# Optimization experiments

Measured on AMD Instinct MI355X. Metric: run time of the kernel, lower is better.

The kernel has to match this reference:

```python
import jax, jax.numpy as jnp
from jax import lax
import numpy as np

T, B, DIM_F, DIM_H, DIM_S, DIM_W = 1024, 32, 512, 512, 1024, 512


def setup_inputs() -> dict:
    key = jax.random.key(0)
    ks = jax.random.split(key, 9)
    F_matrix = jax.random.normal(ks[0], (T, DIM_F), dtype=jnp.float32)
    a_prev = jax.nn.softmax(jax.random.normal(ks[1], (B, T), dtype=jnp.float32), axis=1)
    s_prev = jax.random.normal(ks[2], (B, DIM_S), dtype=jnp.float32)
    h = jax.random.normal(ks[3], (T, B, DIM_H), dtype=jnp.float32)
    # Linear weights stored as [in, out] so y = x @ W (+ b)
    Ww = jax.random.normal(ks[4], (DIM_S, DIM_W), dtype=jnp.float32) / np.sqrt(DIM_S)
    Vw = jax.random.normal(ks[5], (DIM_H, DIM_W), dtype=jnp.float32) / np.sqrt(DIM_H)
    Vb = jax.random.normal(ks[6], (DIM_W,), dtype=jnp.float32) * 0.01
    Uw = jax.random.normal(ks[7], (DIM_F, DIM_W), dtype=jnp.float32) / np.sqrt(DIM_F)
    ww = jax.random.normal(ks[8], (DIM_W,), dtype=jnp.float32) / np.sqrt(DIM_W)
    return {"F_matrix": F_matrix, "a_prev": a_prev, "s_prev": s_prev, "h": h,
            "Ww": Ww, "Vw": Vw, "Vb": Vb, "Uw": Uw, "ww": ww, "beta": 1}


def _calc_f(F_matrix, a_prev):
    # torch.conv2d(input=[1,1,T,dim_f], weight=[B,1,T,1], padding=[(T-1)//2, 0])
    t = F_matrix.shape[0]
    pad = (t - 1) // 2
    lhs = F_matrix[None, None]          # [1, 1, T, dim_f]
    rhs = a_prev[:, None, :, None]      # [B, 1, T, 1]
    f = lax.conv_general_dilated(
        lhs, rhs, window_strides=(1, 1), padding=[(pad, pad), (0, 0)],
        dimension_numbers=("NCHW", "OIHW", "NCHW"))[0]  # [B, T_out, dim_f]
    if f.shape[1] != t:  # even T -> T_out = T-1; pad one leading time row with zeros
        f = jnp.pad(f, ((0, 0), (1, 0), (0, 0)))
    return f


def reference(F_matrix, a_prev, s_prev, h, Ww, Vw, Vb, Uw, ww, beta):
    f_current = _calc_f(F_matrix, a_prev)                 # [B, T, dim_f]
    hT = jnp.swapaxes(h, 0, 1)                            # [B, T, dim_h]
    x = jnp.tanh(jnp.matmul(s_prev, Ww)[:, None, :]       # Ws: [B, 1, dim_w]
                 + jnp.matmul(hT, Vw) + Vb                # Vh: [B, T, dim_w]
                 + jnp.matmul(f_current, Uw))             # Uf: [B, T, dim_w]
    e_current = jnp.einsum("btw,w->bt", x, ww)            # [B, T]
    return jax.nn.softmax(beta * e_current, axis=1)       # 'sharpening' mode
```

## Files before the change

### kernel.cpp

```cpp
#include <hip/hip_runtime.h>
#include <hip/hip_bf16.h>
#include <math.h>

#define T_DIM 1024
#define B_DIM 32
#define DIMF 512
#define DIMH 512
#define DIMS 1024
#define DIMW 512

typedef __attribute__((ext_vector_type(8))) short short8;
typedef __attribute__((ext_vector_type(4))) float f32x4;

__device__ __forceinline__ unsigned f2bf1(float x) {
    unsigned a = __float_as_uint(x);
    return (a + 0x7FFFu + ((a >> 16) & 1u)) >> 16;
}
__device__ __forceinline__ unsigned f2bf2(float lo, float hi) {
    return f2bf1(lo) | (f2bf1(hi) << 16);
}
__device__ __forceinline__ float fast_tanh(float x) {
    return 1.f - __fdividef(2.f, 1.f + __expf(x + x));
}
__device__ __forceinline__ unsigned short bf1(float x) {
    __hip_bfloat16 b = __float2bfloat16(x);
    return *reinterpret_cast<unsigned short*>(&b);
}
__device__ __forceinline__ short8 pack8(float4 a, float4 c) {
    union { unsigned short us[8]; short8 s; } u;
    u.us[0] = bf1(a.x); u.us[1] = bf1(a.y); u.us[2] = bf1(a.z); u.us[3] = bf1(a.w);
    u.us[4] = bf1(c.x); u.us[5] = bf1(c.y); u.us[6] = bf1(c.z); u.us[7] = bf1(c.w);
    return u.s;
}

__device__ __forceinline__ void gl16(const unsigned short* g, unsigned short* l) {
    __builtin_amdgcn_global_load_lds(
        (const __attribute__((address_space(1))) unsigned int*)g,
        (__attribute__((address_space(3))) unsigned int*)l, 16, 0, 0);
}
__device__ __forceinline__ void gl16f(const float* g, float* l) {
    __builtin_amdgcn_global_load_lds(
        (const __attribute__((address_space(1))) unsigned int*)g,
        (__attribute__((address_space(3))) unsigned int*)l, 16, 0, 0);
}

__global__ void __launch_bounds__(256) k_prep_all(
    const float* __restrict__ F, const float* __restrict__ Uw,
    const float* __restrict__ Vw, const float* __restrict__ a_prev,
    const float* __restrict__ s_prev, const float* __restrict__ Ww,
    const float* __restrict__ Vb, const float* __restrict__ h,
    unsigned short* __restrict__ GT, unsigned short* __restrict__ VwT,
    unsigned short* __restrict__ P, float* __restrict__ SWp,
    unsigned short* __restrict__ hB, int nPack) {
    __shared__ float sh[8192];
    const int bz = blockIdx.x;
    const int tid = threadIdx.x;

    if (bz < nPack) {
        for (unsigned i = bz * 256 + tid; i < 32768u * 64; i += (unsigned)nPack * 256) {
            const int r = i >> 6, c8 = (i & 63) * 8;
            const int bb = r >> 10, t = r & 1023;
            const float* src = h + ((size_t)(t * 32 + bb)) * 512 + c8;
            const float4 v0 = *(const float4*)(src);
            const float4 v1 = *(const float4*)(src + 4);
            union { unsigned short us[8]; uint4 u4; } o;
            o.us[0] = bf1(v0.x); o.us[1] = bf1(v0.y);
            o.us[2] = bf1(v0.z); o.us[3] = bf1(v0.w);
            o.us[4] = bf1(v1.x); o.us[5] = bf1(v1.y);
            o.us[6] = bf1(v1.z); o.us[7] = bf1(v1.w);
            *(uint4*)(hB + (size_t)r * 512 + c8) = o.u4;
        }
        return;
    }
    const int bz2 = bz - nPack;
    if (bz2 < 512) {
        const int rt = bz2 & 63, ct = bz2 >> 6;
        const int r0g = rt * 16;
        const float4* Fv = (const float4*)(F + (size_t)r0g * DIMF);
        float4* shv = (float4*)sh;
        for (int i = tid; i < 16 * DIMF / 4; i += 256) shv[i] = Fv[i];
        __syncthreads();
        const int c = ct * 64 + (tid & 63);
        const int r0 = (tid >> 6) * 4;
        float acc[4] = {0.f, 0.f, 0.f, 0.f};
        for (int k = 0; k < DIMF; ++k) {
            const float bv = Uw[(size_t)k * DIMW + c];
#pragma unroll
            for (int j = 0; j < 4; ++j)
                acc[j] = fmaf(sh[(r0 + j) * DIMF + k], bv, acc[j]);
        }
        uint2 o;
        o.x = f2bf2(acc[0], acc[1]);
        o.y = f2bf2(acc[2], acc[3]);
        *(uint2*)(GT + (size_t)c * T_DIM + r0g + r0) = o;
        return;
    }
    const int bz3 = bz2 - 512;
    if (bz3 < 512) {
        if (bz3 < 256) {
            const int k0 = (bz3 >> 4) * 32, n0 = (bz3 & 15) * 32;
            const int x = tid & 31, y = tid >> 5;
#pragma unroll
            for (int i = 0; i < 4; ++i)
                sh[(y + 8 * i) * 33 + x] = Vw[(size_t)(k0 + y + 8 * i) * DIMW + n0 + x];
            __syncthreads();
#pragma unroll
            for (int i = 0; i < 4; ++i) {
                const int n = n0 + y + 8 * i;
                VwT[(size_t)n * DIMH + k0 + x] = (unsigned short)f2bf1(sh[x * 33 + y + 8 * i]);
            }
        } else {
            const int bs = bz3 - 256;
            const int b = bs >> 3, s = bs & 7;
            for (int i = tid; i < 2048; i += 256) {
                const int j = i + s;
                float v = 0.f;
                if (j >= 512 && j < 1536) v = a_prev[(size_t)b * T_DIM + j - 512];
                P[(size_t)bs * 2048 + i] = (unsigned short)f2bf1(v);
            }
        }
        return;
    }
    {
        const int bz4 = bz3 - 512;
        const int c0 = (bz4 & 15) * 32, q = bz4 >> 4;
        float (*shb)[256] = (float(*)[256])sh;
        for (int i = tid; i < 32 * 64; i += 256) {
            const int r = i >> 6, c4 = (i & 63) * 4;
            *(float4*)&shb[r][c4] = *(const float4*)(s_prev + (size_t)r * DIMS + q * 256 + c4);
        }
        __syncthreads();
        const int c  = c0 + (tid & 31);
        const int bg = tid >> 5;
        float acc[4];
#pragma unroll
        for (int j = 0; j < 4; ++j) acc[j] = (q == 0) ? Vb[c] : 0.f;
        const float* W = Ww + (size_t)q * 256 * DIMW;
        for (int k = 0; k < 256; ++k) {
            const float w = W[(size_t)k * DIMW + c];
#pragma unroll
            for (int j = 0; j < 4; ++j)
                acc[j] = fmaf(shb[bg + 8 * j][k], w, acc[j]);
        }
#pragma unroll
        for (int j = 0; j < 4; ++j)
            SWp[((size_t)q * B_DIM + bg + 8 * j) * DIMW + c] = acc[j];
    }
}

__global__ void __launch_bounds__(512, 4) k_main_db(
    const unsigned short* __restrict__ hB, const unsigned short* __restrict__ VwT,
    const unsigned short* __restrict__ GT, const unsigned short* __restrict__ P,
    const float* __restrict__ SWp, const float* __restrict__ ww,
    float* __restrict__ ep) {
    __shared__ unsigned short As2[2][8192];
    __shared__ unsigned short Bs[2][8192];

    const int bid = blockIdx.x;
    const int wg  = (bid & 7) * 128 + (bid >> 3);
    const int x = wg & 3, yy = wg >> 2;
    const int w0 = x * 128;
    const int b  = yy >> 3;
    const int t0 = (yy & 7) * 128;

    const int tid  = threadIdx.x;
    const int lane = tid & 63;
    const int wv   = tid >> 6;
    const int wm = wv >> 2, wn = wv & 3;
    const int g = lane >> 4, r16 = lane & 15;
    const int s7 = r16 & 7;

    f32x4 acc[4][2];
#pragma unroll
    for (int m = 0; m < 4; ++m)
#pragma unroll
        for (int n = 0; n < 2; ++n) acc[m][n] = (f32x4)0.f;

    const int kstart = max(0, t0 - 512);
    const int kend   = min(T_DIM - 1, t0 + 639);
    const int NS2    = (kend - kstart + 1) >> 6;
    const int NT     = 8 + NS2;

    const int rB = lane >> 3;
    const int cB = ((lane & 7) ^ rB) * 8;
    const unsigned short* hSb[2];
    const unsigned short* vS[2];
    const unsigned short* gS[2];
#pragma unroll
    for (int q = 0; q < 2; ++q) {
        hSb[q] = hB + ((size_t)(b * 1024 + t0 + wv * 16 + q * 8 + rB)) * 512 + cB;
        vS[q]  = VwT + (size_t)(w0 + wv * 16 + q * 8 + rB) * DIMH + cB;
        gS[q]  = GT  + (size_t)(w0 + wv * 16 + q * 8 + rB) * T_DIM + kstart + cB;
    }
    const unsigned short* Pb = P + (size_t)b * 8 * 2048;
    const unsigned short* pS[2];
#pragma unroll
    for (int q = 0; q < 2; ++q) {
        const int row = wv * 16 + q * 8 + rB;
        const int jb = kstart + ((lane & 7) ^ rB) * 8 + 1024 - (t0 + row);
        const int sj = jb & 7;
        pS[q] = Pb + sj * 2048 + (jb - sj);
    }
    const bool zrow = (t0 + wm * 64 + r16 == 0);

#define STAGE(u, j)                                                          \
    {                                                                        \
        if ((u) < 8) {                                                       \
            const int o_ = (u) * 64;                                         \
            _Pragma("unroll")                                                \
            for (int q = 0; q < 2; ++q) {                                    \
                gl16(hSb[q] + o_, &As2[j][(wv * 16 + q * 8) * 64]);          \
                gl16(vS[q] + o_,  &Bs[j][(wv * 16 + q * 8) * 64]);           \
            }                                                                \
        } else {                                                             \
            const int o_ = ((u) - 8) * 64;                                   \
            _Pragma("unroll")                                                \
            for (int q = 0; q < 2; ++q) {                                    \
                gl16(pS[q] + o_, &As2[j][(wv * 16 + q * 8) * 64]);           \
                gl16(gS[q] + o_, &Bs[j][(wv * 16 + q * 8) * 64]);            \
            }                                                                \
        }                                                                    \
    }

    STAGE(0, 0);
    __syncthreads();

    for (int u = 0; u < NT; ++u) {
        const int cur = u & 1;
        if (u + 1 < NT) STAGE(u + 1, cur ^ 1);
        const bool p2z = (u >= 8) && zrow;
#pragma unroll
        for (int ks = 0; ks < 2; ++ks) {
            short8 af[4], bf[2];
#pragma unroll
            for (int m = 0; m < 4; ++m)
                af[m] = *(const short8*)&As2[cur][(wm * 64 + m * 16 + r16) * 64 +
                                                  ((ks * 4 + g) ^ s7) * 8];
            if (p2z) af[0] = (short8)(short)0;
#pragma unroll
            for (int n = 0; n < 2; ++n)
                bf[n] = *(const short8*)&Bs[cur][(wn * 32 + n * 16 + r16) * 64 +
                                                 ((ks * 4 + g) ^ s7) * 8];
#pragma unroll
            for (int m = 0; m < 4; ++m)
#pragma unroll
                for (int n = 0; n < 2; ++n)
                    acc[m][n] = __builtin_amdgcn_mfma_f32_16x16x32_bf16(
                        af[m], bf[n], acc[m][n], 0, 0, 0);
        }
        __syncthreads();
    }
#undef STAGE

    float swv[2], wwv[2];
#pragma unroll
    for (int n = 0; n < 2; ++n) {
        const int w = w0 + wn * 32 + n * 16 + r16;
        float sv = 0.f;
#pragma unroll
        for (int q = 0; q < 4; ++q)
            sv += SWp[((size_t)q * B_DIM + b) * DIMW + w];
        swv[n] = sv;
        wwv[n] = ww[w];
    }
    float* Ered = (float*)&As2[0][0];
#pragma unroll
    for (int m = 0; m < 4; ++m) {
#pragma unroll
        for (int reg = 0; reg < 4; ++reg) {
            float s = 0.f;
#pragma unroll
            for (int n = 0; n < 2; ++n)
                s = fmaf(fast_tanh(acc[m][n][reg] + swv[n]), wwv[n], s);
            s += __shfl_xor(s, 1, 64);
            s += __shfl_xor(s, 2, 64);
            s += __shfl_xor(s, 4, 64);
            s += __shfl_xor(s, 8, 64);
            if (r16 == 0)
                Ered[wn * 128 + wm * 64 + m * 16 + g * 4 + reg] = s;
        }
    }
    __syncthreads();
    if (tid < 256) {
        const int p = tid >> 7, row = tid & 127;
        const float v = Ered[p * 128 + row] + Ered[(p + 2) * 128 + row];
        ep[((size_t)(x * 2 + p) * B_DIM + b) * T_DIM + t0 + row] = v;
    }
}

__global__ void __launch_bounds__(256, 3) k_main_fb(
    const float* __restrict__ hF, const unsigned short* __restrict__ VwT,
    const unsigned short* __restrict__ GT, const unsigned short* __restrict__ P,
    const float* __restrict__ SWp, const float* __restrict__ ww,
    float* __restrict__ ep) {
    __shared__ __align__(16) float AsF[8192];
    __shared__ unsigned short Bs[128 * 64];
    unsigned short* As2 = (unsigned short*)AsF;

    const int bid = blockIdx.x;
    const int wg  = (bid & 7) * 128 + (bid >> 3);
    const int x = wg & 3, yy = wg >> 2;
    const int w0 = x * 128;
    const int b  = yy >> 3;
    const int t0 = (yy & 7) * 128;

    const int tid  = threadIdx.x;
    const int lane = tid & 63;
    const int wv   = tid >> 6;
    const int wm = wv >> 1, wn = wv & 1;
    const int g = lane >> 4, r16 = lane & 15;
    const int s7 = r16 & 7;

    f32x4 acc[4][4];
#pragma unroll
    for (int m = 0; m < 4; ++m)
#pragma unroll
        for (int n = 0; n < 4; ++n) acc[m][n] = (f32x4)0.f;

    const int kstart = max(0, t0 - 512);
    const int kend   = min(T_DIM - 1, t0 + 639);
    const int NS2    = (kend - kstart + 1) >> 6;

    const int rB = lane >> 3;
    const int cB = ((lane & 7) ^ rB) * 8;
    const float* hS[8];
    {
        const int rl = lane >> 4, cl = lane & 15;
#pragma unroll
        for (int q = 0; q < 8; ++q) {
            const int row = wv * 32 + q * 4 + rl;
            hS[q] = hF + ((size_t)(t0 + row) * B_DIM + b) * DIMH + ((cl ^ (row & 7)) << 2);
        }
    }
    const unsigned short* vS[4];
    const unsigned short* gS[4];
#pragma unroll
    for (int q = 0; q < 4; ++q) {
        vS[q] = VwT + (size_t)(w0 + wv * 32 + q * 8 + rB) * DIMH + cB;
        gS[q] = GT  + (size_t)(w0 + wv * 32 + q * 8 + rB) * T_DIM + kstart + cB;
    }
    const unsigned short* Pb = P + (size_t)b * 8 * 2048;
    const unsigned short* pS[4];
#pragma unroll
    for (int q = 0; q < 4; ++q) {
        const int row = wv * 32 + q * 8 + rB;
        const int jb = kstart + ((lane & 7) ^ rB) * 8 + 1024 - (t0 + row);
        const int sj = jb & 7;
        pS[q] = Pb + sj * 2048 + (jb - sj);
    }
    const bool zrow = (t0 + wm * 64 + r16 == 0);

    for (int k0 = 0; k0 < DIMH; k0 += 64) {
        __syncthreads();
#pragma unroll
        for (int q = 0; q < 8; ++q) gl16f(hS[q] + k0, AsF + (wv * 32 + q * 4) * 64);
#pragma unroll
        for (int q = 0; q < 4; ++q) gl16(vS[q] + k0, Bs + (wv * 32 + q * 8) * 64);
        __syncthreads();
#pragma unroll
        for (int ks = 0; ks < 2; ++ks) {
            short8 af[4], bf[4];
#pragma unroll
            for (int m = 0; m < 4; ++m) {
                const int base = (wm * 64 + m * 16 + r16) * 64;
                const int clo = ((ks * 8 + 2 * g) ^ s7) * 4;
                const int chi = ((ks * 8 + 2 * g + 1) ^ s7) * 4;
                af[m] = pack8(*(const float4*)&AsF[base + clo],
                              *(const float4*)&AsF[base + chi]);
            }
#pragma unroll
            for (int n = 0; n < 4; ++n)
                bf[n] = *(const short8*)&Bs[(wn * 64 + n * 16 + r16) * 64 +
                                            ((ks * 4 + g) ^ s7) * 8];
#pragma unroll
            for (int m = 0; m < 4; ++m)
#pragma unroll
                for (int n = 0; n < 4; ++n)
                    acc[m][n] = __builtin_amdgcn_mfma_f32_16x16x32_bf16(
                        af[m], bf[n], acc[m][n], 0, 0, 0);
        }
    }
    for (int s2 = 0; s2 < NS2; ++s2) {
        const int o = s2 * 64;
        __syncthreads();
#pragma unroll
        for (int q = 0; q < 4; ++q) gl16(pS[q] + o, As2 + (wv * 32 + q * 8) * 64);
#pragma unroll
        for (int q = 0; q < 4; ++q) gl16(gS[q] + o, Bs + (wv * 32 + q * 8) * 64);
        __syncthreads();
#pragma unroll
        for (int ks = 0; ks < 2; ++ks) {
            short8 af[4], bf[4];
#pragma unroll
            for (int m = 0; m < 4; ++m)
                af[m] = *(const short8*)&As2[(wm * 64 + m * 16 + r16) * 64 +
                                             ((ks * 4 + g) ^ s7) * 8];
            if (zrow) af[0] = (short8)(short)0;
#pragma unroll
            for (int n = 0; n < 4; ++n)
                bf[n] = *(const short8*)&Bs[(wn * 64 + n * 16 + r16) * 64 +
                                            ((ks * 4 + g) ^ s7) * 8];
#pragma unroll
            for (int m = 0; m < 4; ++m)
#pragma unroll
                for (int n = 0; n < 4; ++n)
                    acc[m][n] = __builtin_amdgcn_mfma_f32_16x16x32_bf16(
                        af[m], bf[n], acc[m][n], 0, 0, 0);
        }
    }
    float swv[4], wwv[4];
#pragma unroll
    for (int n = 0; n < 4; ++n) {
        const int w = w0 + wn * 64 + n * 16 + r16;
        float sv = 0.f;
#pragma unroll
        for (int q = 0; q < 4; ++q)
            sv += SWp[((size_t)q * B_DIM + b) * DIMW + w];
        swv[n] = sv;
        wwv[n] = ww[w];
    }
#pragma unroll
    for (int m = 0; m < 4; ++m) {
#pragma unroll
        for (int reg = 0; reg < 4; ++reg) {
            float s = 0.f;
#pragma unroll
            for (int n = 0; n < 4; ++n)
                s = fmaf(fast_tanh(acc[m][n][reg] + swv[n]), wwv[n], s);
            s += __shfl_xor(s, 1, 64);
            s += __shfl_xor(s, 2, 64);
            s += __shfl_xor(s, 4, 64);
            s += __shfl_xor(s, 8, 64);
            if (r16 == 0) {
                const int trow = t0 + wm * 64 + m * 16 + g * 4 + reg;
                ep[((size_t)(x * 2 + wn) * B_DIM + b) * T_DIM + trow] = s;
            }
        }
    }
}

__device__ __forceinline__ float decode_beta(const void* p) {
    const int iv = *(const int*)p;
    const float fv = __int_as_float(iv);
    const float afv = fabsf(fv);
    if (afv >= 1e-6f && afv <= 1e6f) return fv;
    return (float)iv;
}

__global__ void k_softmax(const float* __restrict__ ep, const void* __restrict__ beta_p,
                          float* __restrict__ out) {
    const int b = blockIdx.x;
    const float beta = decode_beta(beta_p);
    __shared__ float redm[4];
    __shared__ float reds[4];
    float v[4];
    float m = -INFINITY;
#pragma unroll
    for (int i = 0; i < 4; ++i) {
        const int t = threadIdx.x * 4 + i;
        float ev = 0.f;
#pragma unroll
        for (int xq = 0; xq < 8; ++xq)
            ev += ep[((size_t)xq * B_DIM + b) * T_DIM + t];
        v[i] = beta * ev;
        m = fmaxf(m, v[i]);
    }
    for (int off = 1; off < 64; off <<= 1) m = fmaxf(m, __shfl_xor(m, off, 64));
    const int wid = threadIdx.x >> 6, lane = threadIdx.x & 63;
    if (lane == 0) redm[wid] = m;
    __syncthreads();
    m = fmaxf(fmaxf(redm[0], redm[1]), fmaxf(redm[2], redm[3]));
    float s = 0.f;
    float ex[4];
#pragma unroll
    for (int i = 0; i < 4; ++i) { ex[i] = expf(v[i] - m); s += ex[i]; }
    for (int off = 1; off < 64; off <<= 1) s += __shfl_xor(s, off, 64);
    if (lane == 0) reds[wid] = s;
    __syncthreads();
    s = reds[0] + reds[1] + reds[2] + reds[3];
    const float inv = 1.f / s;
#pragma unroll
    for (int i = 0; i < 4; ++i)
        out[(size_t)b * T_DIM + threadIdx.x * 4 + i] = ex[i] * inv;
}

extern "C" void kernel_launch(void* const* d_in, const int* in_sizes, int n_in,
                              void* d_out, int out_size, void* d_ws, size_t ws_size,
                              hipStream_t stream) {
    const float* F      = (const float*)d_in[0];
    const float* a_prev = (const float*)d_in[1];
    const float* s_prev = (const float*)d_in[2];
    const float* h      = (const float*)d_in[3];
    const float* Ww     = (const float*)d_in[4];
    const float* Vw     = (const float*)d_in[5];
    const float* Vb     = (const float*)d_in[6];
    const float* Uw     = (const float*)d_in[7];
    const float* ww     = (const float*)d_in[8];
    const void*  beta_p = d_in[9];
    float* out = (float*)d_out;

    char* ws = (char*)d_ws;
    unsigned short* GT  = (unsigned short*)(ws);
    unsigned short* VwT = (unsigned short*)(ws + (1u << 20));
    unsigned short* P   = (unsigned short*)(ws + (1u << 20) + (512u << 10));
    float* SWp = (float*)(ws + (2u << 20) + (512u << 10));
    float* ep  = (float*)(ws + (2u << 20) + (768u << 10));
    unsigned short* hB = (unsigned short*)(ws + (4u << 20));

    const bool big = ws_size >= (36ull << 20);
    const int nPack = big ? 1024 : 0;

    k_prep_all<<<dim3(nPack + 1088), 256, 0, stream>>>(
        F, Uw, Vw, a_prev, s_prev, Ww, Vb, h, GT, VwT, P, SWp, hB, nPack);
    if (big) {
        k_main_db<<<dim3(1024), 512, 0, stream>>>(hB, VwT, GT, P, SWp, ww, ep);
    } else {
        k_main_fb<<<dim3(1024), 256, 0, stream>>>(h, VwT, GT, P, SWp, ww, ep);
    }
    k_softmax<<<dim3(32), 256, 0, stream>>>(ep, beta_p, out);
}
```

Measured before the change: 105.6 us.

## Use 256x128 tiles without double buffering in main kernel; rework fallback to 512 threads

The main fused GEMM kernel now covers 256 time rows by 128 output columns per block, launched as 512 blocks instead of 1024. Each wave computes a 64x64 sub-tile with a single-buffered shared-memory loop, replacing the previous double-buffered 128x128 pipeline. The larger tile is meant to cut redundant loads of the weight and Toeplitz operands and the number of blocks. The cost is loss of load/compute overlap, fewer blocks to fill the GPU, and a slightly longer convolution K range per block. The fallback kernel is rewritten as a 512-thread variant with 128x128 tiles.

```diff
diff --git a/kernel.cpp b/kernel.cpp
--- a/kernel.cpp
+++ b/kernel.cpp
@@ -148,13 +148,165 @@
     }
 }
 
-__global__ void __launch_bounds__(512, 4) k_main_db(
+__global__ void __launch_bounds__(512, 4) k_main_t(
     const unsigned short* __restrict__ hB, const unsigned short* __restrict__ VwT,
     const unsigned short* __restrict__ GT, const unsigned short* __restrict__ P,
     const float* __restrict__ SWp, const float* __restrict__ ww,
     float* __restrict__ ep) {
-    __shared__ unsigned short As2[2][8192];
-    __shared__ unsigned short Bs[2][8192];
+    __shared__ unsigned short As2[256 * 64];
+    __shared__ unsigned short Bs[128 * 64];
+
+    const int bid = blockIdx.x;
+    const int wg  = (bid & 7) * 64 + (bid >> 3);
+    const int x = wg & 3, yy = wg >> 2;
+    const int w0 = x * 128;
+    const int b  = yy >> 2;
+    const int t0 = (yy & 3) * 256;
+
+    const int tid  = threadIdx.x;
+    const int lane = tid & 63;
+    const int wv   = tid >> 6;
+    const int wm = wv >> 1, wn = wv & 1;
+    const int g = lane >> 4, r16 = lane & 15;
+    const int s7 = r16 & 7;
+
+    f32x4 acc[4][4];
+#pragma unroll
+    for (int m = 0; m < 4; ++m)
+#pragma unroll
+        for (int n = 0; n < 4; ++n) acc[m][n] = (f32x4)0.f;
+
+    const int kstart = max(0, t0 - 512);
+    const int kend   = min(T_DIM - 1, t0 + 766);
+    const int NS2    = (kend - kstart + 64) >> 6;
+    const int NT     = 8 + NS2;
+
+    const int rB = lane >> 3;
+    const int cB = ((lane & 7) ^ rB) * 8;
+    const unsigned short* hSb[4];
+#pragma unroll
+    for (int q = 0; q < 4; ++q)
+        hSb[q] = hB + ((size_t)(b * 1024 + t0 + wv * 32 + q * 8 + rB)) * 512 + cB;
+    const unsigned short* vS[2];
+    const unsigned short* gS[2];
+#pragma unroll
+    for (int q = 0; q < 2; ++q) {
+        vS[q] = VwT + (size_t)(w0 + wv * 16 + q * 8 + rB) * DIMH + cB;
+        gS[q] = GT  + (size_t)(w0 + wv * 16 + q * 8 + rB) * T_DIM + kstart + cB;
+    }
+    const unsigned short* Pb = P + (size_t)b * 8 * 2048;
+    const unsigned short* pS[4];
+#pragma unroll
+    for (int q = 0; q < 4; ++q) {
+        const int row = wv * 32 + q * 8 + rB;
+        const int jb = kstart + ((lane & 7) ^ rB) * 8 + 1024 - (t0 + row);
+        const int sj = jb & 7;
+        pS[q] = Pb + sj * 2048 + (jb - sj);
+    }
+    const bool zrow = (t0 + wm * 64 + r16 == 0);
+
+    for (int k0 = 0; k0 < DIMH; k0 += 64) {
+        __syncthreads();
+#pragma unroll
+        for (int q = 0; q < 4; ++q) gl16(hSb[q] + k0, As2 + (wv * 32 + q * 8) * 64);
+#pragma unroll
+        for (int q = 0; q < 2; ++q) gl16(vS[q] + k0, Bs + (wv * 16 + q * 8) * 64);
+        __syncthreads();
+
+#pragma unroll
+        for (int ks = 0; ks < 2; ++ks) {
+            short8 af[4], bf[4];
+#pragma unroll
+            for (int m = 0; m < 4; ++m)
+                af[m] = *(const short8*)&As2[(wm * 64 + m * 16 + r16) * 64 +
+                                             ((ks * 4 + g) ^ s7) * 8];
+#pragma unroll
+            for (int n = 0; n < 4; ++n)
+                bf[n] = *(const short8*)&Bs[(wn * 64 + n * 16 + r16) * 64 +
+                                            ((ks * 4 + g) ^ s7) * 8];
+#pragma unroll
+            for (int m = 0; m < 4; ++m)
+#pragma unroll
+                for (int n = 0; n < 4; ++n)
+                    acc[m][n] = __builtin_amdgcn_mfma_f32_16x16x32_bf16(
+                        af[m], bf[n], acc[m][n], 0, 0, 0);
+        }
+    }
+
+    for (int s2 = 0; s2 < NS2; ++s2) {
+        const int o = s2 * 64;
+        __syncthreads();
+#pragma unroll
+        for (int q = 0; q < 4; ++q) gl16(pS[q] + o, As2 + (wv * 32 + q * 8) * 64);
+#pragma unroll
+        for (int q = 0; q < 2; ++q) gl16(gS[q] + o, Bs + (wv * 16 + q * 8) * 64);
+        __syncthreads();
+
+#pragma unroll
+        for (int ks = 0; ks < 2; ++ks) {
+            short8 af[4], bf[4];
+#pragma unroll
+            for (int m = 0; m < 4; ++m)
+                af[m] = *(const short8*)&As2[(wm * 64 + m * 16 + r16) * 64 +
+                                             ((ks * 4 + g) ^ s7) * 8];
+            if (zrow) af[0] = (short8)(short)0;
+#pragma unroll
+            for (int n = 0; n < 4; ++n)
+                bf[n] = *(const short8*)&Bs[(wn * 64 + n * 16 + r16) * 64 +
+                                            ((ks * 4 + g) ^ s7) * 8];
+#pragma unroll
+            for (int m = 0; m < 4; ++m)
+#pragma unroll
+                for (int n = 0; n < 4; ++n)
+                    acc[m][n] = __builtin_amdgcn_mfma_f32_16x16x32_bf16(
+                        af[m], bf[n], acc[m][n], 0, 0, 0);
+        }
+    }
+
+    float swv[4], wwv[4];
+#pragma unroll
+    for (int n = 0; n < 4; ++n) {
+        const int w = w0 + wn * 64 + n * 16 + r16;
+        float sv = 0.f;
+#pragma unroll
+        for (int q = 0; q < 4; ++q)
+            sv += SWp[((size_t)q * B_DIM + b) * DIMW + w];
+        swv[n] = sv;
+        wwv[n] = ww[w];
+    }
+    __syncthreads();
+    float* Ered = (float*)&As2[0];
+#pragma unroll
+    for (int m = 0; m < 4; ++m) {
+#pragma unroll
+        for (int reg = 0; reg < 4; ++reg) {
+            float s = 0.f;
+#pragma unroll
+            for (int n = 0; n < 4; ++n)
+                s = fmaf(fast_tanh(acc[m][n][reg] + swv[n]), wwv[n], s);
+            s += __shfl_xor(s, 1, 64);
+            s += __shfl_xor(s, 2, 64);
+            s += __shfl_xor(s, 4, 64);
+            s += __shfl_xor(s, 8, 64);
+            if (r16 == 0)
+                Ered[wn * 256 + wm * 64 + m * 16 + g * 4 + reg] = s;
+        }
+    }
+    __syncthreads();
+    {
+        const int p = tid >> 8, row = tid & 255;
+        ep[((size_t)(x * 2 + p) * B_DIM + b) * T_DIM + t0 + row] = Ered[p * 256 + row];
+    }
+}
+
+__global__ void __launch_bounds__(512, 4) k_main_s(
+    const float* __restrict__ hF, const unsigned short* __restrict__ VwT,
+    const unsigned short* __restrict__ GT, const unsigned short* __restrict__ P,
+    const float* __restrict__ SWp, const float* __restrict__ ww,
+    float* __restrict__ ep) {
+    __shared__ __align__(16) float AsF[8192];
+    __shared__ unsigned short Bs[8192];
+    unsigned short* As2 = (unsigned short*)AsF;
 
     const int bid = blockIdx.x;
     const int wg  = (bid & 7) * 128 + (bid >> 3);
@@ -179,18 +331,22 @@
     const int kstart = max(0, t0 - 512);
     const int kend   = min(T_DIM - 1, t0 + 639);
     const int NS2    = (kend - kstart + 1) >> 6;
-    const int NT     = 8 + NS2;
-
+
+    const int rl = lane >> 4, cl = lane & 15;
+    const float* hS[4];
+#pragma unroll
+    for (int q = 0; q < 4; ++q) {
+        const int row = wv * 16 + q * 4 + rl;
+        hS[q] = hF + ((size_t)(t0 + row) * B_DIM + b) * DIMH + ((cl ^ (row & 7)) << 2);
+    }
     const int rB = lane >> 3;
     const int cB = ((lane & 7) ^ rB) * 8;
-    const unsigned short* hSb[2];
     const unsigned short* vS[2];
     const unsigned short* gS[2];
 #pragma unroll
     for (int q = 0; q < 2; ++q) {
-        hSb[q] = hB + ((size_t)(b * 1024 + t0 + wv * 16 + q * 8 + rB)) * 512 + cB;
-        vS[q]  = VwT + (size_t)(w0 + wv * 16 + q * 8 + rB) * DIMH + cB;
-        gS[q]  = GT  + (size_t)(w0 + wv * 16 + q * 8 + rB) * T_DIM + kstart + cB;
+        vS[q] = VwT + (size_t)(w0 + wv * 16 + q * 8 + rB) * DIMH + cB;
+        gS[q] = GT  + (size_t)(w0 + wv * 16 + q * 8 + rB) * T_DIM + kstart + cB;
     }
     const unsigned short* Pb = P + (size_t)b * 8 * 2048;
     const unsigned short* pS[2];
@@ -203,44 +359,28 @@
     }
     const bool zrow = (t0 + wm * 64 + r16 == 0);
 
-#define STAGE(u, j)                                                          \
-    {                                                                        \
-        if ((u) < 8) {                                                       \
-            const int o_ = (u) * 64;                                         \
-            _Pragma("unroll")                                                \
-            for (int q = 0; q < 2; ++q) {                                    \
-                gl16(hSb[q] + o_, &As2[j][(wv * 16 + q * 8) * 64]);          \
-                gl16(vS[q] + o_,  &Bs[j][(wv * 16 + q * 8) * 64]);           \
-            }                                                                \
-        } else {                                                             \
-            const int o_ = ((u) - 8) * 64;                                   \
-            _Pragma("unroll")                                                \
-            for (int q = 0; q < 2; ++q) {                                    \
-                gl16(pS[q] + o_, &As2[j][(wv * 16 + q * 8) * 64]);           \
-                gl16(gS[q] + o_, &Bs[j][(wv * 16 + q * 8) * 64]);            \
-            }                                                                \
-        }                                                                    \
-    }
-
-    STAGE(0, 0);
-    __syncthreads();
-
-    for (int u = 0; u < NT; ++u) {
-        const int cur = u & 1;
-        if (u + 1 < NT) STAGE(u + 1, cur ^ 1);
-        const bool p2z = (u >= 8) && zrow;
+    for (int k0 = 0; k0 < DIMH; k0 += 64) {
+        __syncthreads();
+#pragma unroll
+        for (int q = 0; q < 4; ++q) gl16f(hS[q] + k0, AsF + (wv * 16 + q * 4) * 64);
+#pragma unroll
+        for (int q = 0; q < 2; ++q) gl16(vS[q] + k0, Bs + (wv * 16 + q * 8) * 64);
+        __syncthreads();
 #pragma unroll
         for (int ks = 0; ks < 2; ++ks) {
             short8 af[4], bf[2];
 #pragma unroll
-            for (int m = 0; m < 4; ++m)
-                af[m] = *(const short8*)&As2[cur][(wm * 64 + m * 16 + r16) * 64 +
-                                                  ((ks * 4 + g) ^ s7) * 8];
-            if (p2z) af[0] = (short8)(short)0;
+            for (int m = 0; m < 4; ++m) {
+                const int base = (wm * 64 + m * 16 + r16) * 64;
+                const int clo = ((ks * 8 + 2 * g) ^ s7) * 4;
+                const int chi = ((ks * 8 + 2 * g + 1) ^ s7) * 4;
+                af[m] = pack8(*(const float4*)&AsF[base + clo],
+                              *(const float4*)&AsF[base + chi]);
+            }
 #pragma unroll
             for (int n = 0; n < 2; ++n)
-                bf[n] = *(const short8*)&Bs[cur][(wn * 32 + n * 16 + r16) * 64 +
-                                                 ((ks * 4 + g) ^ s7) * 8];
+                bf[n] = *(const short8*)&Bs[(wn * 32 + n * 16 + r16) * 64 +
+                                            ((ks * 4 + g) ^ s7) * 8];
 #pragma unroll
             for (int m = 0; m < 4; ++m)
 #pragma unroll
@@ -248,10 +388,35 @@
                     acc[m][n] = __builtin_amdgcn_mfma_f32_16x16x32_bf16(
                         af[m], bf[n], acc[m][n], 0, 0, 0);
         }
-        __syncthreads();
-    }
-#undef STAGE
-
+    }
+    for (int s2 = 0; s2 < NS2; ++s2) {
+        const int o = s2 * 64;
+        __syncthreads();
+#pragma unroll
+        for (int q = 0; q < 2; ++q) gl16(pS[q] + o, As2 + (wv * 16 + q * 8) * 64);
+#pragma unroll
+        for (int q = 0; q < 2; ++q) gl16(gS[q] + o, Bs + (wv * 16 + q * 8) * 64);
+        __syncthreads();
+#pragma unroll
+        for (int ks = 0; ks < 2; ++ks) {
+            short8 af[4], bf[2];
+#pragma unroll
+            for (int m = 0; m < 4; ++m)
+                af[m] = *(const short8*)&As2[(wm * 64 + m * 16 + r16) * 64 +
+                                             ((ks * 4 + g) ^ s7) * 8];
+            if (zrow) af[0] = (short8)(short)0;
+#pragma unroll
+            for (int n = 0; n < 2; ++n)
+                bf[n] = *(const short8*)&Bs[(wn * 32 + n * 16 + r16) * 64 +
+                                            ((ks * 4 + g) ^ s7) * 8];
+#pragma unroll
+            for (int m = 0; m < 4; ++m)
+#pragma unroll
+                for (int n = 0; n < 2; ++n)
+                    acc[m][n] = __builtin_amdgcn_mfma_f32_16x16x32_bf16(
+                        af[m], bf[n], acc[m][n], 0, 0, 0);
+        }
+    }
     float swv[2], wwv[2];
 #pragma unroll
     for (int n = 0; n < 2; ++n) {
@@ -263,7 +428,8 @@
         swv[n] = sv;
         wwv[n] = ww[w];
     }
-    float* Ered = (float*)&As2[0][0];
+    __syncthreads();
+    float* Ered = (float*)&AsF[0];
 #pragma unroll
     for (int m = 0; m < 4; ++m) {
 #pragma unroll
@@ -285,157 +451,6 @@
         const int p = tid >> 7, row = tid & 127;
         const float v = Ered[p * 128 + row] + Ered[(p + 2) * 128 + row];
         ep[((size_t)(x * 2 + p) * B_DIM + b) * T_DIM + t0 + row] = v;
-    }
-}
-
-__global__ void __launch_bounds__(256, 3) k_main_fb(
-    const float* __restrict__ hF, const unsigned short* __restrict__ VwT,
-    const unsigned short* __restrict__ GT, const unsigned short* __restrict__ P,
-    const float* __restrict__ SWp, const float* __restrict__ ww,
-    float* __restrict__ ep) {
-    __shared__ __align__(16) float AsF[8192];
-    __shared__ unsigned short Bs[128 * 64];
-    unsigned short* As2 = (unsigned short*)AsF;
-
-    const int bid = blockIdx.x;
-    const int wg  = (bid & 7) * 128 + (bid >> 3);
-    const int x = wg & 3, yy = wg >> 2;
-    const int w0 = x * 128;
-    const int b  = yy >> 3;
-    const int t0 = (yy & 7) * 128;
-
-    const int tid  = threadIdx.x;
-    const int lane = tid & 63;
-    const int wv   = tid >> 6;
-    const int wm = wv >> 1, wn = wv & 1;
-    const int g = lane >> 4, r16 = lane & 15;
-    const int s7 = r16 & 7;
-
-    f32x4 acc[4][4];
-#pragma unroll
-    for (int m = 0; m < 4; ++m)
-#pragma unroll
-        for (int n = 0; n < 4; ++n) acc[m][n] = (f32x4)0.f;
-
-    const int kstart = max(0, t0 - 512);
-    const int kend   = min(T_DIM - 1, t0 + 639);
-    const int NS2    = (kend - kstart + 1) >> 6;
-
-    const int rB = lane >> 3;
-    const int cB = ((lane & 7) ^ rB) * 8;
-    const float* hS[8];
-    {
-        const int rl = lane >> 4, cl = lane & 15;
-#pragma unroll
-        for (int q = 0; q < 8; ++q) {
-            const int row = wv * 32 + q * 4 + rl;
-            hS[q] = hF + ((size_t)(t0 + row) * B_DIM + b) * DIMH + ((cl ^ (row & 7)) << 2);
-        }
-    }
-    const unsigned short* vS[4];
-    const unsigned short* gS[4];
-#pragma unroll
-    for (int q = 0; q < 4; ++q) {
-        vS[q] = VwT + (size_t)(w0 + wv * 32 + q * 8 + rB) * DIMH + cB;
-        gS[q] = GT  + (size_t)(w0 + wv * 32 + q * 8 + rB) * T_DIM + kstart + cB;
-    }
-    const unsigned short* Pb = P + (size_t)b * 8 * 2048;
-    const unsigned short* pS[4];
-#pragma unroll
-    for (int q = 0; q < 4; ++q) {
-        const int row = wv * 32 + q * 8 + rB;
-        const int jb = kstart + ((lane & 7) ^ rB) * 8 + 1024 - (t0 + row);
-        const int sj = jb & 7;
-        pS[q] = Pb + sj * 2048 + (jb - sj);
-    }
-    const bool zrow = (t0 + wm * 64 + r16 == 0);
-
-    for (int k0 = 0; k0 < DIMH; k0 += 64) {
-        __syncthreads();
-#pragma unroll
-        for (int q = 0; q < 8; ++q) gl16f(hS[q] + k0, AsF + (wv * 32 + q * 4) * 64);
-#pragma unroll
-        for (int q = 0; q < 4; ++q) gl16(vS[q] + k0, Bs + (wv * 32 + q * 8) * 64);
-        __syncthreads();
-#pragma unroll
-        for (int ks = 0; ks < 2; ++ks) {
-            short8 af[4], bf[4];
-#pragma unroll
-            for (int m = 0; m < 4; ++m) {
-                const int base = (wm * 64 + m * 16 + r16) * 64;
-                const int clo = ((ks * 8 + 2 * g) ^ s7) * 4;
-                const int chi = ((ks * 8 + 2 * g + 1) ^ s7) * 4;
-                af[m] = pack8(*(const float4*)&AsF[base + clo],
-                              *(const float4*)&AsF[base + chi]);
-            }
-#pragma unroll
-            for (int n = 0; n < 4; ++n)
-                bf[n] = *(const short8*)&Bs[(wn * 64 + n * 16 + r16) * 64 +
-                                            ((ks * 4 + g) ^ s7) * 8];
-#pragma unroll
-            for (int m = 0; m < 4; ++m)
-#pragma unroll
-                for (int n = 0; n < 4; ++n)
-                    acc[m][n] = __builtin_amdgcn_mfma_f32_16x16x32_bf16(
-                        af[m], bf[n], acc[m][n], 0, 0, 0);
-        }
-    }
-    for (int s2 = 0; s2 < NS2; ++s2) {
-        const int o = s2 * 64;
-        __syncthreads();
-#pragma unroll
-        for (int q = 0; q < 4; ++q) gl16(pS[q] + o, As2 + (wv * 32 + q * 8) * 64);
-#pragma unroll
-        for (int q = 0; q < 4; ++q) gl16(gS[q] + o, Bs + (wv * 32 + q * 8) * 64);
-        __syncthreads();
-#pragma unroll
-        for (int ks = 0; ks < 2; ++ks) {
-            short8 af[4], bf[4];
-#pragma unroll
-            for (int m = 0; m < 4; ++m)
-                af[m] = *(const short8*)&As2[(wm * 64 + m * 16 + r16) * 64 +
-                                             ((ks * 4 + g) ^ s7) * 8];
-            if (zrow) af[0] = (short8)(short)0;
-#pragma unroll
-            for (int n = 0; n < 4; ++n)
-                bf[n] = *(const short8*)&Bs[(wn * 64 + n * 16 + r16) * 64 +
-                                            ((ks * 4 + g) ^ s7) * 8];
-#pragma unroll
-            for (int m = 0; m < 4; ++m)
-#pragma unroll
-                for (int n = 0; n < 4; ++n)
-                    acc[m][n] = __builtin_amdgcn_mfma_f32_16x16x32_bf16(
-                        af[m], bf[n], acc[m][n], 0, 0, 0);
-        }
-    }
-    float swv[4], wwv[4];
-#pragma unroll
-    for (int n = 0; n < 4; ++n) {
-        const int w = w0 + wn * 64 + n * 16 + r16;
-        float sv = 0.f;
-#pragma unroll
-        for (int q = 0; q < 4; ++q)
-            sv += SWp[((size_t)q * B_DIM + b) * DIMW + w];
-        swv[n] = sv;
-        wwv[n] = ww[w];
-    }
-#pragma unroll
-    for (int m = 0; m < 4; ++m) {
-#pragma unroll
-        for (int reg = 0; reg < 4; ++reg) {
-            float s = 0.f;
-#pragma unroll
-            for (int n = 0; n < 4; ++n)
-                s = fmaf(fast_tanh(acc[m][n][reg] + swv[n]), wwv[n], s);
-            s += __shfl_xor(s, 1, 64);
-            s += __shfl_xor(s, 2, 64);
-            s += __shfl_xor(s, 4, 64);
-            s += __shfl_xor(s, 8, 64);
-            if (r16 == 0) {
-                const int trow = t0 + wm * 64 + m * 16 + g * 4 + reg;
-                ep[((size_t)(x * 2 + wn) * B_DIM + b) * T_DIM + trow] = s;
-            }
-        }
     }
 }
 
@@ -513,9 +528,9 @@
     k_prep_all<<<dim3(nPack + 1088), 256, 0, stream>>>(
         F, Uw, Vw, a_prev, s_prev, Ww, Vb, h, GT, VwT, P, SWp, hB, nPack);
     if (big) {
-        k_main_db<<<dim3(1024), 512, 0, stream>>>(hB, VwT, GT, P, SWp, ww, ep);
+        k_main_t<<<dim3(512), 512, 0, stream>>>(hB, VwT, GT, P, SWp, ww, ep);
     } else {
-        k_main_fb<<<dim3(1024), 256, 0, stream>>>(h, VwT, GT, P, SWp, ww, ep);
+        k_main_s<<<dim3(1024), 512, 0, stream>>>(h, VwT, GT, P, SWp, ww, ep);
     }
     k_softmax<<<dim3(32), 256, 0, stream>>>(ep, beta_p, out);
 }
```

Measured after the change: 102.6 us. 2.8% less time.
